# Kernel tuning notes

Measured on AMD Instinct MI355X. Metric: run time of the kernel, lower is better.

Reference implementation:

```python
import jax, jax.numpy as jnp
import numpy as np

N, E, F, H, G = 50000, 1600000, 128, 128, 64
EPS = 1e-5  # BatchNorm eps


def setup_inputs() -> dict:
    key = jax.random.key(0)
    ks = jax.random.split(key, 16)
    x = jax.random.normal(ks[0], (N, F), dtype=jnp.float32)
    edge_index = jax.random.randint(ks[1], (2, E), 0, N, dtype=jnp.int64)
    batch = jnp.sort(jax.random.randint(ks[2], (N,), 0, G, dtype=jnp.int64))
    inp = {
        'x': x, 'edge_index': edge_index, 'batch': batch,
        'W1': jax.random.normal(ks[3], (F, H), dtype=jnp.float32) / np.sqrt(F),
        'b1': jnp.zeros((H,), jnp.float32),
        'bn1_gamma': jax.random.uniform(ks[4], (H,), jnp.float32, 0.5, 1.5),
        'bn1_beta': jax.random.normal(ks[5], (H,), jnp.float32) * 0.1,
        'bn1_mean': jax.random.normal(ks[6], (H,), jnp.float32) * 0.1,
        'bn1_var': jax.random.uniform(ks[7], (H,), jnp.float32, 0.5, 1.5),
        'W2': jax.random.normal(ks[8], (H, H), dtype=jnp.float32) / np.sqrt(H),
        'b2': jnp.zeros((H,), jnp.float32),
        'bn2_gamma': jax.random.uniform(ks[9], (H,), jnp.float32, 0.5, 1.5),
        'bn2_beta': jax.random.normal(ks[10], (H,), jnp.float32) * 0.1,
        'bn2_mean': jax.random.normal(ks[11], (H,), jnp.float32) * 0.1,
        'bn2_var': jax.random.uniform(ks[12], (H,), jnp.float32, 0.5, 1.5),
        'att_w': jax.random.normal(ks[13], (H, 1), dtype=jnp.float32) / np.sqrt(H),
        'cls_w': jax.random.normal(ks[14], (1, H), dtype=jnp.float32) / np.sqrt(H),
        'cls_b': jnp.zeros((1,), jnp.float32),
    }
    return inp


def gcn_conv(h, W, b, src, dst, n):
    # PyG GCNConv: linear, add self-loops, symmetric D^{-1/2}(A+I)D^{-1/2} aggregation, bias.
    hw = h @ W                                   # [n, H]
    loops = jnp.arange(n, dtype=src.dtype)
    s = jnp.concatenate([src, loops])
    d = jnp.concatenate([dst, loops])
    deg = jax.ops.segment_sum(jnp.ones_like(d, dtype=hw.dtype), d, num_segments=n)
    dis = jnp.where(deg > 0, jax.lax.rsqrt(deg), 0.0)
    norm = dis[s] * dis[d]                       # [E+n]
    msgs = hw[s] * norm[:, None]                 # gather + scale (memory-bound)
    return jax.ops.segment_sum(msgs, d, num_segments=n) + b


def batch_norm(h, gamma, beta, mean, var):
    return (h - mean) * gamma * jax.lax.rsqrt(var + EPS) + beta


def reference(x, edge_index, batch, W1, b1, bn1_gamma, bn1_beta, bn1_mean, bn1_var,
              W2, b2, bn2_gamma, bn2_beta, bn2_mean, bn2_var, att_w, cls_w, cls_b):
    n = x.shape[0]
    src, dst = edge_index[0], edge_index[1]
    # eval mode: dropout and edge-dropout are no-ops; BN uses running stats
    h = gcn_conv(x, W1, b1, src, dst, n)
    h = jax.nn.relu(batch_norm(h, bn1_gamma, bn1_beta, bn1_mean, bn1_var))
    h = gcn_conv(h, W2, b2, src, dst, n)
    h = jax.nn.relu(batch_norm(h, bn2_gamma, bn2_beta, bn2_mean, bn2_var))
    att = jax.nn.sigmoid(h @ att_w)              # [n, 1]
    g = jax.ops.segment_sum(h * att, batch, num_segments=G)  # [G, H]
    logits = g @ cls_w.T + cls_b                 # [G, 1]
    return logits, att
```

## Files before the change

### kernel.cpp

```cpp
#include <hip/hip_runtime.h>
#include <math.h>

#define NN 50000
#define HID 128
#define NG 64
#define BN_EPS 1e-5f

typedef __attribute__((ext_vector_type(8))) short short8;
typedef __attribute__((ext_vector_type(4))) float f32x4;

__device__ inline unsigned pack_bf2(float a, float b) {
    union { float f; unsigned u; } ua, ub;
    ua.f = a; ub.f = b;
    unsigned x = ua.u, y = ub.u;
    x += 0x7fffu + ((x >> 16) & 1u);
    y += 0x7fffu + ((y >> 16) & 1u);
    return (x >> 16) | (y & 0xffff0000u);
}
__device__ inline unsigned short bf16_1(float x) {
    union { float f; unsigned u; } v;
    v.f = x;
    unsigned r = v.u + 0x7fffu + ((v.u >> 16) & 1u);
    return (unsigned short)(r >> 16);
}
__device__ inline float2 unpack_bf2(unsigned v) {
    union { unsigned u; float f; } a, b;
    a.u = v << 16;
    b.u = v & 0xffff0000u;
    return make_float2(a.f, b.f);
}

#define NBKT 256
#define ETILE 2048
#define EPT   (ETILE / 256)
#define CAP   8192
#define ASTR 136

__global__ __launch_bounds__(128) void k_prep0(const float* __restrict__ W1,
                                               const float* __restrict__ W2,
                                               unsigned short* __restrict__ wt1,
                                               unsigned short* __restrict__ wt2,
                                               int* __restrict__ bcurP,
                                               const float* __restrict__ cls_b,
                                               float* __restrict__ logits) {
    int b = blockIdx.x;
    int t = threadIdx.x;
    if (b < 256) {
        int k = b & 127;
        const float* W = (b < 128) ? W1 : W2;
        unsigned short* wt = (b < 128) ? wt1 : wt2;
        wt[t * 128 + k] = bf16_1(W[k * 128 + t]);
    } else {
        #pragma unroll
        for (int i = 0; i < 32; ++i) bcurP[t * 32 + i] = 0;
        if (t < NG) logits[t] = cls_b[0];
    }
}

__global__ __launch_bounds__(256) void k_distribute(const int* __restrict__ src,
                                                    const int* __restrict__ dst,
                                                    int* __restrict__ bcurP,
                                                    unsigned* __restrict__ bpacked,
                                                    int E, int K) {
    __shared__ int h[NBKT];
    int t = threadIdx.x;
    h[t] = 0;
    __syncthreads();
    int base = blockIdx.x * ETILE;
    int dreg[EPT];
    #pragma unroll
    for (int i = 0; i < EPT; ++i) {
        int e = base + i * 256 + t;
        dreg[i] = (e < E) ? dst[e] : -1;
        if (dreg[i] >= 0) atomicAdd(&h[dreg[i] / K], 1);
    }
    __syncthreads();
    int c = h[t];
    int my = (c > 0) ? atomicAdd(&bcurP[t * 16], c) : 0;
    __syncthreads();
    h[t] = my;
    __syncthreads();
    #pragma unroll
    for (int i = 0; i < EPT; ++i) {
        int e = base + i * 256 + t;
        if (dreg[i] >= 0) {
            int d = dreg[i];
            int bkt = d / K;
            int p = atomicAdd(&h[bkt], 1);
            bpacked[(size_t)bkt * CAP + p] = ((unsigned)d << 16) | (unsigned)src[e];
        }
    }
}

__global__ __launch_bounds__(256) void k_csr_gemm1(const unsigned* __restrict__ bpacked,
                                                   const int* __restrict__ bcurP,
                                                   int* __restrict__ row_ptr,
                                                   int* __restrict__ degA,
                                                   float* __restrict__ dis,
                                                   int* __restrict__ col_idx,
                                                   const float* __restrict__ x,
                                                   const unsigned short* __restrict__ wt1,
                                                   unsigned short* __restrict__ zb,
                                                   int n, int K) {
    __shared__ unsigned short A[64][ASTR];
    __shared__ int cnt[NBKT];
    __shared__ int sA[NBKT];
    __shared__ int cur[NBKT];
    int t = threadIdx.x;
    int b = blockIdx.x;

    if (b >= NBKT) {
        int row0 = (b - NBKT) * 64;
        #pragma unroll
        for (int i = 0; i < 8; ++i) {
            int idx = t + i * 256;
            int r = idx >> 5;
            int c4 = (idx & 31) * 4;
            float4 v = make_float4(0.f, 0.f, 0.f, 0.f);
            if (row0 + r < n) v = *(const float4*)&x[(size_t)(row0 + r) * 128 + c4];
            uint2 p;
            p.x = pack_bf2(v.x, v.y);
            p.y = pack_bf2(v.z, v.w);
            *(uint2*)&A[r][c4] = p;
        }
        __syncthreads();
        int lane = t & 63;
        int wave = t >> 6;
        int m = lane & 15;
        int quad = lane >> 4;
        int r0 = wave * 16;
        short8 a[4];
        #pragma unroll
        for (int kt = 0; kt < 4; ++kt)
            a[kt] = *(const short8*)&A[r0 + m][kt * 32 + quad * 8];
        f32x4 acc[8];
        #pragma unroll
        for (int ct = 0; ct < 8; ++ct) acc[ct] = (f32x4){0.f, 0.f, 0.f, 0.f};
        short8 bcur[4], bnxt[4];
        {
            const unsigned short* wb = &wt1[(size_t)m * 128 + quad * 8];
            #pragma unroll
            for (int kt = 0; kt < 4; ++kt) bcur[kt] = *(const short8*)(wb + kt * 32);
        }
        #pragma unroll
        for (int ct = 0; ct < 8; ++ct) {
            if (ct < 7) {
                const unsigned short* wb = &wt1[(size_t)((ct + 1) * 16 + m) * 128 + quad * 8];
                #pragma unroll
                for (int kt = 0; kt < 4; ++kt) bnxt[kt] = *(const short8*)(wb + kt * 32);
            }
            #pragma unroll
            for (int kt = 0; kt < 4; ++kt)
                acc[ct] = __builtin_amdgcn_mfma_f32_16x16x32_bf16(a[kt], bcur[kt], acc[ct], 0, 0, 0);
            #pragma unroll
            for (int kt = 0; kt < 4; ++kt) bcur[kt] = bnxt[kt];
        }
        __syncthreads();
        #pragma unroll
        for (int ct = 0; ct < 8; ++ct) {
            int col = ct * 16 + m;
            #pragma unroll
            for (int reg = 0; reg < 4; ++reg)
                A[r0 + quad * 4 + reg][col] = bf16_1(acc[ct][reg]);
        }
        __syncthreads();
        #pragma unroll
        for (int i = 0; i < 4; ++i) {
            int idx = t + i * 256;
            int r = idx >> 4;
            int c8 = (idx & 15) * 8;
            int grow = row0 + r;
            if (grow < n)
                *(uint4*)&zb[(size_t)grow * 128 + c8] = *(const uint4*)&A[r][c8];
        }
        return;
    }

    int node0 = b * K;
    int nn = n - node0;
    if (nn > K) nn = K;
    if (nn < 0) nn = 0;
    int e0 = b * CAP;
    int e1 = e0 + bcurP[b * 16];
    cnt[t] = 0;
    __syncthreads();
    for (int e = e0 + t; e < e1; e += 256) {
        int ld = (int)(bpacked[e] >> 16) - node0;
        atomicAdd(&cnt[ld], 1);
    }
    __syncthreads();
    int c = cnt[t];
    sA[t] = c;
    __syncthreads();
    for (int off = 1; off < NBKT; off <<= 1) {
        int v = (t >= off) ? sA[t - off] : 0;
        __syncthreads();
        sA[t] += v;
        __syncthreads();
    }
    int rp = e0 + sA[t] - c;
    cur[t] = rp;
    if (t < nn) {
        row_ptr[node0 + t] = rp;
        degA[node0 + t] = c;
        dis[node0 + t] = rsqrtf((float)(c + 1));
    }
    __syncthreads();
    for (int e = e0 + t; e < e1; e += 256) {
        unsigned v = bpacked[e];
        int ld = (int)(v >> 16) - node0;
        int p = atomicAdd(&cur[ld], 1);
        col_idx[p] = (int)(v & 0xFFFFu);
    }
}


__device__ inline void gather4wide(const unsigned short* __restrict__ hwsb,
                                   const int* __restrict__ col_idx,
                                   int e0, int deg, int md,
                                   int sl, int part, bool active,
                                   float* acc8) {
    int cidx = (active && sl < deg) ? col_idx[e0 + sl] : 0;
    for (int it0 = 0; it0 < md; it0 += 16) {
        int nx = it0 + 16;
        int cidx_next = (active && (nx + sl) < deg && nx < md) ? col_idx[e0 + nx + sl] : 0;
        uint4 vv[16];
        #pragma unroll
        for (int j = 0; j < 16; ++j) {
            int s = __shfl(cidx, (part << 4) + j);
            vv[j] = (it0 + j < deg)
                        ? *(const uint4*)(hwsb + ((size_t)s << 7) + (sl << 3))
                        : make_uint4(0, 0, 0, 0);
        }
        #pragma unroll
        for (int j = 0; j < 16; ++j) {
            const unsigned* w = (const unsigned*)&vv[j];
            #pragma unroll
            for (int i2 = 0; i2 < 4; ++i2) {
                float2 f = unpack_bf2(w[i2]);
                acc8[2 * i2]     += f.x;
                acc8[2 * i2 + 1] += f.y;
            }
        }
        cidx = cidx_next;
    }
}

__device__ inline void gather4wide_scaled(const unsigned short* __restrict__ zb,
                                          const int* __restrict__ col_idx,
                                          const float* __restrict__ dis,
                                          int e0, int deg, int md,
                                          int sl, int part, bool active,
                                          float* acc8) {
    int cidx = (active && sl < deg) ? col_idx[e0 + sl] : 0;
    float cdis = (active && sl < deg) ? dis[cidx] : 0.f;
    for (int it0 = 0; it0 < md; it0 += 16) {
        int nx = it0 + 16;
        bool okn = (active && (nx + sl) < deg && nx < md);
        int cidx_next = okn ? col_idx[e0 + nx + sl] : 0;
        float cdis_next = okn ? dis[cidx_next] : 0.f;
        uint4 vv[16];
        float dsj[16];
        #pragma unroll
        for (int j = 0; j < 16; ++j) {
            int s = __shfl(cidx, (part << 4) + j);
            dsj[j] = __shfl(cdis, (part << 4) + j);
            vv[j] = (it0 + j < deg)
                        ? *(const uint4*)(zb + ((size_t)s << 7) + (sl << 3))
                        : make_uint4(0, 0, 0, 0);
        }
        #pragma unroll
        for (int j = 0; j < 16; ++j) {
            const unsigned* w = (const unsigned*)&vv[j];
            #pragma unroll
            for (int i2 = 0; i2 < 4; ++i2) {
                float2 f = unpack_bf2(w[i2]);
                acc8[2 * i2]     = fmaf(f.x, dsj[j], acc8[2 * i2]);
                acc8[2 * i2 + 1] = fmaf(f.y, dsj[j], acc8[2 * i2 + 1]);
            }
        }
        cidx = cidx_next;
        cdis = cdis_next;
    }
}


__global__ __launch_bounds__(256) void k_agg1_gemm2(const unsigned short* __restrict__ zb,
                                                    const int* __restrict__ row_ptr,
                                                    const int* __restrict__ degA,
                                                    const int* __restrict__ col_idx,
                                                    const float* __restrict__ dis,
                                                    const float* __restrict__ bias,
                                                    const float* __restrict__ gamma,
                                                    const float* __restrict__ beta,
                                                    const float* __restrict__ mean,
                                                    const float* __restrict__ var,
                                                    const unsigned short* __restrict__ wt2,
                                                    unsigned short* __restrict__ hwsb2, int n) {
    __shared__ unsigned short H1[16][ASTR];
    __shared__ unsigned short C2[16][ASTR];
    int t = threadIdx.x;
    int wave = t >> 6, lane = t & 63;
    int sl = lane & 15, part = lane >> 4;
    int d = blockIdx.x * 16 + wave * 4 + part;
    bool active = (d < n);
    int e0 = 0, deg = 0;
    if (active) {
        e0 = row_ptr[d];
        deg = degA[d];
    }
    int md = deg;
    md = max(md, __shfl_xor(md, 16));
    md = max(md, __shfl_xor(md, 32));

    float acc8[8] = {0, 0, 0, 0, 0, 0, 0, 0};
    gather4wide_scaled(zb, col_idx, dis, e0, deg, md, sl, part, active, acc8);

    unsigned outw[4] = {0, 0, 0, 0};
    if (active) {
        float dd = dis[d];
        uint4 v = *(const uint4*)(zb + ((size_t)d << 7) + (sl << 3));
        const unsigned* w = (const unsigned*)&v;
        #pragma unroll
        for (int i2 = 0; i2 < 4; ++i2) {
            float2 f = unpack_bf2(w[i2]);
            acc8[2 * i2]     = fmaf(f.x, dd, acc8[2 * i2]);
            acc8[2 * i2 + 1] = fmaf(f.y, dd, acc8[2 * i2 + 1]);
        }
        int f0 = sl << 3;
        #pragma unroll
        for (int i2 = 0; i2 < 4; ++i2) {
            int f = f0 + 2 * i2;
            float2 bv = *(const float2*)&bias[f];
            float2 gm = *(const float2*)&gamma[f];
            float2 bt = *(const float2*)&beta[f];
            float2 mn = *(const float2*)&mean[f];
            float2 vr = *(const float2*)&var[f];
            float vx = acc8[2 * i2] * dd + bv.x;
            float vy = acc8[2 * i2 + 1] * dd + bv.y;
            float sx = gm.x * rsqrtf(vr.x + BN_EPS);
            float sy = gm.y * rsqrtf(vr.y + BN_EPS);
            float rx = fmaxf((vx - mn.x) * sx + bt.x, 0.f);
            float ry = fmaxf((vy - mn.y) * sy + bt.y, 0.f);
            outw[i2] = pack_bf2(rx, ry);
        }
    }
    int local = wave * 4 + part;
    *(uint4*)&H1[local][sl << 3] = *(uint4*)outw;
    __syncthreads();

    int m = sl;
    int quad = part;
    short8 a2[4];
    #pragma unroll
    for (int kt = 0; kt < 4; ++kt)
        a2[kt] = *(const short8*)&H1[m][kt * 32 + quad * 8];

    f32x4 acc2[2];
    acc2[0] = (f32x4){0.f, 0.f, 0.f, 0.f};
    acc2[1] = (f32x4){0.f, 0.f, 0.f, 0.f};
    #pragma unroll
    for (int i = 0; i < 2; ++i) {
        int ct = wave * 2 + i;
        const unsigned short* wb = &wt2[(size_t)(ct * 16 + m) * 128 + quad * 8];
        #pragma unroll
        for (int kt = 0; kt < 4; ++kt) {
            short8 b = *(const short8*)(wb + kt * 32);
            acc2[i] = __builtin_amdgcn_mfma_f32_16x16x32_bf16(a2[kt], b, acc2[i], 0, 0, 0);
        }
    }
    int gr = blockIdx.x * 16 + quad * 4;
    float ds2[4];
    #pragma unroll
    for (int reg = 0; reg < 4; ++reg)
        ds2[reg] = (gr + reg < n) ? dis[gr + reg] : 0.f;
    #pragma unroll
    for (int i = 0; i < 2; ++i) {
        int col = (wave * 2 + i) * 16 + m;
        #pragma unroll
        for (int reg = 0; reg < 4; ++reg)
            C2[quad * 4 + reg][col] = bf16_1(acc2[i][reg] * ds2[reg]);
    }
    __syncthreads();
    {
        int r = t >> 4;
        int c8 = (t & 15) * 8;
        int grow = blockIdx.x * 16 + r;
        if (grow < n)
            *(uint4*)&hwsb2[(size_t)grow * 128 + c8] = *(const uint4*)&C2[r][c8];
    }
}


__global__ __launch_bounds__(256) void k_agg2_att_logit(const unsigned short* __restrict__ hwsb,
                                                        const int* __restrict__ row_ptr,
                                                        const int* __restrict__ degA,
                                                        const int* __restrict__ col_idx,
                                                        const float* __restrict__ dis,
                                                        const float* __restrict__ bias,
                                                        const float* __restrict__ gamma,
                                                        const float* __restrict__ beta,
                                                        const float* __restrict__ mean,
                                                        const float* __restrict__ var,
                                                        const int* __restrict__ batch,
                                                        const float* __restrict__ att_w,
                                                        const float* __restrict__ cls_w,
                                                        float* __restrict__ att_out,
                                                        float* __restrict__ logits, int n) {
    __shared__ int   sg[16];
    __shared__ float sv[16];
    int t = threadIdx.x;
    int wave = t >> 6, lane = t & 63;
    int sl = lane & 15, part = lane >> 4;
    int d = blockIdx.x * 16 + wave * 4 + part;
    bool active = (d < n);
    int e0 = 0, deg = 0;
    if (active) {
        e0 = row_ptr[d];
        deg = degA[d];
    }
    int md = deg;
    md = max(md, __shfl_xor(md, 16));
    md = max(md, __shfl_xor(md, 32));

    float acc8[8] = {0, 0, 0, 0, 0, 0, 0, 0};
    gather4wide(hwsb, col_idx, e0, deg, md, sl, part, active, acc8);

    int g = -1;
    float contrib = 0.f;
    float p = 0.f, q = 0.f;
    if (active) {
        uint4 v = *(const uint4*)(hwsb + ((size_t)d << 7) + (sl << 3));
        const unsigned* w = (const unsigned*)&v;
        #pragma unroll
        for (int i2 = 0; i2 < 4; ++i2) {
            float2 f = unpack_bf2(w[i2]);
            acc8[2 * i2]     += f.x;
            acc8[2 * i2 + 1] += f.y;
        }
        float dd = dis[d];
        int f0 = sl << 3;
        #pragma unroll
        for (int i2 = 0; i2 < 4; ++i2) {
            int f = f0 + 2 * i2;
            float2 bv = *(const float2*)&bias[f];
            float2 gm = *(const float2*)&gamma[f];
            float2 bt = *(const float2*)&beta[f];
            float2 mn = *(const float2*)&mean[f];
            float2 vr = *(const float2*)&var[f];
            float vx = acc8[2 * i2] * dd + bv.x;
            float vy = acc8[2 * i2 + 1] * dd + bv.y;
            float sx = gm.x * rsqrtf(vr.x + BN_EPS);
            float sy = gm.y * rsqrtf(vr.y + BN_EPS);
            float rx = fmaxf((vx - mn.x) * sx + bt.x, 0.f);
            float ry = fmaxf((vy - mn.y) * sy + bt.y, 0.f);
            float2 aw = *(const float2*)&att_w[f];
            float2 cw = *(const float2*)&cls_w[f];
            p += rx * aw.x + ry * aw.y;
            q += rx * cw.x + ry * cw.y;
        }
    }
    #pragma unroll
    for (int off = 1; off < 16; off <<= 1) {
        p += __shfl_xor(p, off);
        q += __shfl_xor(q, off);
    }
    if (active) {
        float a = 1.f / (1.f + expf(-p));
        if (sl == 0) att_out[d] = a;
        g = batch[d];
        contrib = a * q;
    }
    if (sl == 0) {
        sg[wave * 4 + part] = g;
        sv[wave * 4 + part] = contrib;
    }
    __syncthreads();
    if (t == 0) {
        int cur = -1;
        float acc = 0.f;
        #pragma unroll
        for (int i = 0; i < 16; ++i) {
            int gi = sg[i];
            if (gi < 0) continue;
            if (gi != cur) {
                if (cur >= 0) atomicAdd(&logits[cur], acc);
                cur = gi;
                acc = 0.f;
            }
            acc += sv[i];
        }
        if (cur >= 0) atomicAdd(&logits[cur], acc);
    }
}


extern "C" void kernel_launch(void* const* d_in, const int* in_sizes, int n_in,
                              void* d_out, int out_size, void* d_ws, size_t ws_size,
                              hipStream_t stream) {
    const float* x   = (const float*)d_in[0];
    const int*   ei  = (const int*)d_in[1];
    const int*   bat = (const int*)d_in[2];
    const float* W1  = (const float*)d_in[3];
    const float* b1  = (const float*)d_in[4];
    const float* g1  = (const float*)d_in[5];
    const float* bt1 = (const float*)d_in[6];
    const float* mn1 = (const float*)d_in[7];
    const float* vr1 = (const float*)d_in[8];
    const float* W2  = (const float*)d_in[9];
    const float* b2  = (const float*)d_in[10];
    const float* g2  = (const float*)d_in[11];
    const float* bt2 = (const float*)d_in[12];
    const float* mn2 = (const float*)d_in[13];
    const float* vr2 = (const float*)d_in[14];
    const float* attw = (const float*)d_in[15];
    const float* clsw = (const float*)d_in[16];
    const float* clsb = (const float*)d_in[17];

    int E = in_sizes[1] / 2;
    int n = in_sizes[2];
    const int* src = ei;
    const int* dst = ei + E;
    int K = (n + NBKT - 1) / NBKT;

    char* ws = (char*)d_ws;
    auto alloc = [&](size_t bytes) {
        void* p = (void*)ws;
        ws += (bytes + 255) & ~(size_t)255;
        return p;
    };
    int*            bcurP   = (int*)alloc(NBKT * 16 * 4);
    unsigned*       bpacked = (unsigned*)alloc((size_t)NBKT * CAP * 4);
    int*            row_ptr = (int*)alloc((size_t)n * 4);
    int*            degA    = (int*)alloc((size_t)n * 4);
    int*            col_idx = (int*)alloc((size_t)NBKT * CAP * 4);
    float*          dis     = (float*)alloc((size_t)n * 4);
    unsigned short* zb      = (unsigned short*)alloc((size_t)n * 128 * 2);
    unsigned short* hwsb2   = (unsigned short*)alloc((size_t)n * 128 * 2);
    unsigned short* wt1     = (unsigned short*)alloc(128 * 128 * 2);
    unsigned short* wt2     = (unsigned short*)alloc(128 * 128 * 2);

    float* out = (float*)d_out;
    int etiles = (E + ETILE - 1) / ETILE;
    int gb = (n + 63) / 64;
    int ab = (n + 15) / 16;

    k_prep0<<<257, 128, 0, stream>>>(W1, W2, wt1, wt2, bcurP, clsb, out);
    k_distribute<<<etiles, 256, 0, stream>>>(src, dst, bcurP, bpacked, E, K);
    k_csr_gemm1<<<NBKT + gb, 256, 0, stream>>>(bpacked, bcurP, row_ptr, degA, dis,
                                               col_idx, x, wt1, zb, n, K);
    k_agg1_gemm2<<<ab, 256, 0, stream>>>(zb, row_ptr, degA, col_idx, dis,
                                         b1, g1, bt1, mn1, vr1, wt2, hwsb2, n);
    k_agg2_att_logit<<<ab, 256, 0, stream>>>(hwsb2, row_ptr, degA, col_idx, dis,
                                             b2, g2, bt2, mn2, vr2, bat, attw, clsw,
                                             out + NG, out, n);
}
```

Measured before the change: 282.4 us.

## Double-buffer neighbor gathers with vectorized padded col_idx loads

```diff
diff --git a/kernel.cpp b/kernel.cpp
--- a/kernel.cpp
+++ b/kernel.cpp
@@ -190,7 +190,8 @@
     }
     __syncthreads();
     int c = cnt[t];
-    sA[t] = c;
+    int cp4 = (c + 3) & ~3;
+    sA[t] = cp4;
     __syncthreads();
     for (int off = 1; off < NBKT; off <<= 1) {
         int v = (t >= off) ? sA[t - off] : 0;
@@ -198,7 +199,7 @@
         sA[t] += v;
         __syncthreads();
     }
-    int rp = e0 + sA[t] - c;
+    int rp = e0 + sA[t] - cp4;
     cur[t] = rp;
     if (t < nn) {
         row_ptr[node0 + t] = rp;
@@ -215,88 +216,102 @@
 }
 
 
-__device__ inline void gather4wide(const unsigned short* __restrict__ hwsb,
-                                   const int* __restrict__ col_idx,
-                                   int e0, int deg, int md,
-                                   int sl, int part, bool active,
-                                   float* acc8) {
-    int cidx = (active && sl < deg) ? col_idx[e0 + sl] : 0;
-    for (int it0 = 0; it0 < md; it0 += 16) {
-        int nx = it0 + 16;
-        int cidx_next = (active && (nx + sl) < deg && nx < md) ? col_idx[e0 + nx + sl] : 0;
-        uint4 vv[16];
-        #pragma unroll
-        for (int j = 0; j < 16; ++j) {
-            int s = __shfl(cidx, (part << 4) + j);
-            vv[j] = (it0 + j < deg)
-                        ? *(const uint4*)(hwsb + ((size_t)s << 7) + (sl << 3))
-                        : make_uint4(0, 0, 0, 0);
-        }
-        #pragma unroll
-        for (int j = 0; j < 16; ++j) {
-            const unsigned* w = (const unsigned*)&vv[j];
-            #pragma unroll
-            for (int i2 = 0; i2 < 4; ++i2) {
-                float2 f = unpack_bf2(w[i2]);
+#define GT 8
+
+template<bool SCALED>
+__device__ __forceinline__ void gather_tile_idx(const int* __restrict__ col_idx,
+                                                const float* __restrict__ dis,
+                                                int e0, int deg, int it0,
+                                                int* s, float* ds) {
+    const uint4* cp = (const uint4*)(col_idx + e0 + it0);
+    uint4 c0 = cp[0];
+    uint4 c1 = cp[1];
+    s[0] = c0.x; s[1] = c0.y; s[2] = c0.z; s[3] = c0.w;
+    s[4] = c1.x; s[5] = c1.y; s[6] = c1.z; s[7] = c1.w;
+    if (SCALED) {
+        #pragma unroll
+        for (int j = 0; j < GT; ++j)
+            ds[j] = (it0 + j < deg) ? dis[s[j]] : 0.f;
+    }
+}
+
+__device__ __forceinline__ void gather_tile_rows(const unsigned short* __restrict__ hws,
+                                                 int deg, int it0, int sl,
+                                                 const int* s, uint4* v) {
+    #pragma unroll
+    for (int j = 0; j < GT; ++j)
+        v[j] = (it0 + j < deg)
+                   ? *(const uint4*)(hws + ((size_t)s[j] << 7) + (sl << 3))
+                   : make_uint4(0, 0, 0, 0);
+}
+
+template<bool SCALED>
+__device__ __forceinline__ void gather_consume(const uint4* v, const float* ds, float* acc8) {
+    #pragma unroll
+    for (int j = 0; j < GT; ++j) {
+        const unsigned* w = (const unsigned*)&v[j];
+        #pragma unroll
+        for (int i2 = 0; i2 < 4; ++i2) {
+            float2 f = unpack_bf2(w[i2]);
+            if (SCALED) {
+                acc8[2 * i2]     = fmaf(f.x, ds[j], acc8[2 * i2]);
+                acc8[2 * i2 + 1] = fmaf(f.y, ds[j], acc8[2 * i2 + 1]);
+            } else {
                 acc8[2 * i2]     += f.x;
                 acc8[2 * i2 + 1] += f.y;
             }
         }
-        cidx = cidx_next;
-    }
-}
-
-__device__ inline void gather4wide_scaled(const unsigned short* __restrict__ zb,
-                                          const int* __restrict__ col_idx,
-                                          const float* __restrict__ dis,
-                                          int e0, int deg, int md,
-                                          int sl, int part, bool active,
-                                          float* acc8) {
-    int cidx = (active && sl < deg) ? col_idx[e0 + sl] : 0;
-    float cdis = (active && sl < deg) ? dis[cidx] : 0.f;
-    for (int it0 = 0; it0 < md; it0 += 16) {
-        int nx = it0 + 16;
-        bool okn = (active && (nx + sl) < deg && nx < md);
-        int cidx_next = okn ? col_idx[e0 + nx + sl] : 0;
-        float cdis_next = okn ? dis[cidx_next] : 0.f;
-        uint4 vv[16];
-        float dsj[16];
-        #pragma unroll
-        for (int j = 0; j < 16; ++j) {
-            int s = __shfl(cidx, (part << 4) + j);
-            dsj[j] = __shfl(cdis, (part << 4) + j);
-            vv[j] = (it0 + j < deg)
-                        ? *(const uint4*)(zb + ((size_t)s << 7) + (sl << 3))
-                        : make_uint4(0, 0, 0, 0);
-        }
-        #pragma unroll
-        for (int j = 0; j < 16; ++j) {
-            const unsigned* w = (const unsigned*)&vv[j];
-            #pragma unroll
-            for (int i2 = 0; i2 < 4; ++i2) {
-                float2 f = unpack_bf2(w[i2]);
-                acc8[2 * i2]     = fmaf(f.x, dsj[j], acc8[2 * i2]);
-                acc8[2 * i2 + 1] = fmaf(f.y, dsj[j], acc8[2 * i2 + 1]);
-            }
-        }
-        cidx = cidx_next;
-        cdis = cdis_next;
-    }
-}
-
-
-__global__ __launch_bounds__(256) void k_agg1_gemm2(const unsigned short* __restrict__ zb,
-                                                    const int* __restrict__ row_ptr,
-                                                    const int* __restrict__ degA,
-                                                    const int* __restrict__ col_idx,
-                                                    const float* __restrict__ dis,
-                                                    const float* __restrict__ bias,
-                                                    const float* __restrict__ gamma,
-                                                    const float* __restrict__ beta,
-                                                    const float* __restrict__ mean,
-                                                    const float* __restrict__ var,
-                                                    const unsigned short* __restrict__ wt2,
-                                                    unsigned short* __restrict__ hwsb2, int n) {
+    }
+}
+
+template<bool SCALED>
+__device__ __forceinline__ void gather_pipe(const unsigned short* __restrict__ hws,
+                                            const int* __restrict__ col_idx,
+                                            const float* __restrict__ dis,
+                                            int e0, int deg, int md, int sl,
+                                            float* acc8) {
+    int nt = (md + GT - 1) / GT;
+    if (nt <= 0) return;
+    int sA[GT], sB[GT];
+    float dA[GT], dB[GT];
+    uint4 vA[GT], vB[GT];
+    gather_tile_idx<SCALED>(col_idx, dis, e0, deg, 0, sA, dA);
+    gather_tile_rows(hws, deg, 0, sl, sA, vA);
+    int t = 0;
+    for (;;) {
+        if (t + 1 < nt) {
+            gather_tile_idx<SCALED>(col_idx, dis, e0, deg, (t + 1) * GT, sB, dB);
+            gather_tile_rows(hws, deg, (t + 1) * GT, sl, sB, vB);
+            gather_consume<SCALED>(vA, dA, acc8);
+        } else {
+            gather_consume<SCALED>(vA, dA, acc8);
+            break;
+        }
+        if (t + 2 < nt) {
+            gather_tile_idx<SCALED>(col_idx, dis, e0, deg, (t + 2) * GT, sA, dA);
+            gather_tile_rows(hws, deg, (t + 2) * GT, sl, sA, vA);
+            gather_consume<SCALED>(vB, dB, acc8);
+        } else {
+            gather_consume<SCALED>(vB, dB, acc8);
+            break;
+        }
+        t += 2;
+    }
+}
+
+
+__global__ __launch_bounds__(256, 3) void k_agg1_gemm2(const unsigned short* __restrict__ zb,
+                                                       const int* __restrict__ row_ptr,
+                                                       const int* __restrict__ degA,
+                                                       const int* __restrict__ col_idx,
+                                                       const float* __restrict__ dis,
+                                                       const float* __restrict__ bias,
+                                                       const float* __restrict__ gamma,
+                                                       const float* __restrict__ beta,
+                                                       const float* __restrict__ mean,
+                                                       const float* __restrict__ var,
+                                                       const unsigned short* __restrict__ wt2,
+                                                       unsigned short* __restrict__ hwsb2, int n) {
     __shared__ unsigned short H1[16][ASTR];
     __shared__ unsigned short C2[16][ASTR];
     int t = threadIdx.x;
@@ -314,7 +329,7 @@
     md = max(md, __shfl_xor(md, 32));
 
     float acc8[8] = {0, 0, 0, 0, 0, 0, 0, 0};
-    gather4wide_scaled(zb, col_idx, dis, e0, deg, md, sl, part, active, acc8);
+    gather_pipe<true>(zb, col_idx, dis, e0, deg, md, sl, acc8);
 
     unsigned outw[4] = {0, 0, 0, 0};
     if (active) {
@@ -392,21 +407,21 @@
 }
 
 
-__global__ __launch_bounds__(256) void k_agg2_att_logit(const unsigned short* __restrict__ hwsb,
-                                                        const int* __restrict__ row_ptr,
-                                                        const int* __restrict__ degA,
-                                                        const int* __restrict__ col_idx,
-                                                        const float* __restrict__ dis,
-                                                        const float* __restrict__ bias,
-                                                        const float* __restrict__ gamma,
-                                                        const float* __restrict__ beta,
-                                                        const float* __restrict__ mean,
-                                                        const float* __restrict__ var,
-                                                        const int* __restrict__ batch,
-                                                        const float* __restrict__ att_w,
-                                                        const float* __restrict__ cls_w,
-                                                        float* __restrict__ att_out,
-                                                        float* __restrict__ logits, int n) {
+__global__ __launch_bounds__(256, 3) void k_agg2_att_logit(const unsigned short* __restrict__ hwsb,
+                                                           const int* __restrict__ row_ptr,
+                                                           const int* __restrict__ degA,
+                                                           const int* __restrict__ col_idx,
+                                                           const float* __restrict__ dis,
+                                                           const float* __restrict__ bias,
+                                                           const float* __restrict__ gamma,
+                                                           const float* __restrict__ beta,
+                                                           const float* __restrict__ mean,
+                                                           const float* __restrict__ var,
+                                                           const int* __restrict__ batch,
+                                                           const float* __restrict__ att_w,
+                                                           const float* __restrict__ cls_w,
+                                                           float* __restrict__ att_out,
+                                                           float* __restrict__ logits, int n) {
     __shared__ int   sg[16];
     __shared__ float sv[16];
     int t = threadIdx.x;
@@ -424,7 +439,7 @@
     md = max(md, __shfl_xor(md, 32));
 
     float acc8[8] = {0, 0, 0, 0, 0, 0, 0, 0};
-    gather4wide(hwsb, col_idx, e0, deg, md, sl, part, active, acc8);
+    gather_pipe<false>(hwsb, col_idx, dis, e0, deg, md, sl, acc8);
 
     int g = -1;
     float contrib = 0.f;
@@ -533,7 +548,7 @@
     unsigned*       bpacked = (unsigned*)alloc((size_t)NBKT * CAP * 4);
     int*            row_ptr = (int*)alloc((size_t)n * 4);
     int*            degA    = (int*)alloc((size_t)n * 4);
-    int*            col_idx = (int*)alloc((size_t)NBKT * CAP * 4);
+    int*            col_idx = (int*)alloc(((size_t)NBKT * CAP + 1024) * 4);
     float*          dis     = (float*)alloc((size_t)n * 4);
     unsigned short* zb      = (unsigned short*)alloc((size_t)n * 128 * 2);
     unsigned short* hwsb2   = (unsigned short*)alloc((size_t)n * 128 * 2);
```

Measured after the change: 312.3 us. +10.6%, slower.
